# Optimization experiments

Hardware: AMD Instinct MI355X
Metric: run time of the kernel (lower is better)

## Reference

```python
import jax, jax.numpy as jnp
import numpy as np

N, F, DEG, C = 20000, 64, 16, 16   # nodes, features, in-degree incl. self loop, classes
E = N * (DEG - 1)                   # regular (non-self-loop) edges


def setup_inputs() -> dict:
    key = jax.random.key(0)
    ks = jax.random.split(key, 12)
    x = jax.random.normal(ks[0], (N, F), dtype=jnp.float32)
    src = jax.random.randint(ks[1], (E,), 0, N, dtype=jnp.int32)
    dst = jnp.repeat(jnp.arange(N, dtype=jnp.int32), DEG - 1)  # exactly DEG-1 in-edges/node
    edge_index = jnp.stack([src, dst])
    s = 1.0 / np.sqrt(F)
    params = {}
    for i, kw, kb in ((1, ks[2], ks[3]), (2, ks[4], ks[5]), (3, ks[6], ks[7])):
        params[f"W{i}"] = jax.random.normal(kw, (F, F), dtype=jnp.float32) * s
        params[f"b{i}"] = jax.random.normal(kb, (F,), dtype=jnp.float32) * s
    params["Wfc"] = jax.random.normal(ks[8], (C, F), dtype=jnp.float32) * s
    params["bfc"] = jax.random.normal(ks[9], (C,), dtype=jnp.float32) * s
    return {"x": x, "edge_index": edge_index, **params}


def _pca_conv(h, src, dst, W, b):
    # GCNConv.forward: linear first, then propagate with symmetric normalization.
    hl = h @ W.T                                             # [N, F]
    # add self loops (appended after regular edges, as in PyG)
    loop = jnp.arange(N, dtype=src.dtype)
    src_a = jnp.concatenate([src, loop])
    dst_a = jnp.concatenate([dst, loop])
    deg = jnp.zeros((N,), hl.dtype).at[dst_a].add(1.0)
    dinv = jax.lax.rsqrt(deg)
    norm = dinv[src_a] * dinv[dst_a]                         # [Ea]
    m = norm[:, None] * hl[src_a]                            # messages [Ea, F]
    # aggregate(): pack each destination's messages contiguously, in edge order
    order = jnp.argsort(dst_a)                               # stable sort by destination
    sd = dst_a[order]
    slot = jnp.arange(sd.shape[0]) - jnp.searchsorted(sd, sd, side='left')
    neigh = jnp.zeros((N, DEG, F), hl.dtype).at[sd, slot].set(m[order])
    neigh = neigh.reshape(N, DEG * F)                        # [N, max_degree*F]
    # torch.pca_lowrank(neigh, q=F, center=True): top-F right singular vectors of
    # the column-centered matrix; computed via eigh on the (DEG*F x DEG*F) Gram.
    Xc = neigh - jnp.mean(neigh, axis=0, keepdims=True)
    G = Xc.T @ Xc                                            # [DEG*F, DEG*F]
    _, V = jnp.linalg.eigh(G)                                # ascending eigenvalues
    Vtop = V[:, ::-1][:, :F]                                 # top-F principal directions
    proj = neigh @ Vtop                                      # note: projects UNcentered neigh
    return proj @ W.T + b                                    # self.lin again + bias


def reference(x, edge_index, W1, b1, W2, b2, W3, b3, Wfc, bfc):
    src, dst = edge_index[0], edge_index[1]
    h = jax.nn.relu(_pca_conv(x, src, dst, W1, b1))
    h = jax.nn.relu(_pca_conv(h, src, dst, W2, b2))
    h = jax.nn.relu(_pca_conv(h, src, dst, W3, b3))
    out = h @ Wfc.T + bfc
    return jax.nn.log_softmax(out, axis=-1)
```

## Files before the change

kernel.cpp:

```cpp
#include <hip/hip_runtime.h>
#include <cmath>

#define NNODES 20000
#define FD 64
#define EPN 15
#define NB 1024
#define BSUB 80
#define NCLS 16

__global__ __launch_bounds__(256) void k_linT(const float* __restrict__ X,
    const float* __restrict__ W, const float* __restrict__ bias,
    float* __restrict__ out, int ncol, int relu)
{
  __shared__ float Wsh[64][65];
  __shared__ float Xsh[64][65];
  int t = threadIdx.x;
  int r0 = blockIdx.x * 64;
  for (int idx = t; idx < ncol * 64; idx += 256) Wsh[idx >> 6][idx & 63] = W[idx];
  for (int idx = t; idx < 64 * 64; idx += 256) {
    int r = idx >> 6, c = idx & 63;
    Xsh[r][c] = (r0 + r < NNODES) ? X[(size_t)(r0 + r) * 64 + c] : 0.f;
  }
  __syncthreads();
  for (int idx = t; idx < 64 * ncol; idx += 256) {
    int r = idx / ncol, o = idx % ncol;
    float acc = 0.f;
    #pragma unroll
    for (int j = 0; j < 64; j++) acc += Xsh[r][j] * Wsh[o][j];
    if (bias) acc += bias[o];
    if (relu) acc = fmaxf(acc, 0.f);
    if (r0 + r < NNODES) out[(size_t)(r0 + r) * ncol + o] = acc;
  }
}

__global__ __launch_bounds__(256) void k_meanslot(const float* __restrict__ hl,
    const int* __restrict__ src, float* __restrict__ mus)
{
  int k = blockIdx.x;
  int part = blockIdx.y;
  int t = threadIdx.x;
  int c = t & 63, sub = t >> 6;
  int d0 = part * 2500;
  float acc = 0.f;
  for (int d = d0 + sub; d < d0 + 2500; d += 4) {
    int row = (k < EPN) ? src[d * EPN + k] : d;
    acc += hl[(size_t)row * 64 + c];
  }
  __shared__ float red[4][64];
  red[sub][c] = acc;
  __syncthreads();
  if (t < 64) {
    float s = red[0][t] + red[1][t] + red[2][t] + red[3][t];
    atomicAdd(&mus[k * 64 + t], s * (1.f / 20000.f));
  }
}

__global__ __launch_bounds__(256) void k_gram(const float* __restrict__ hl,
    const int* __restrict__ src, const float* __restrict__ mus,
    float* __restrict__ T)
{
  __shared__ float Ash[64][64];
  __shared__ float Bsh[64][64];
  __shared__ float muA[64], muB[64];
  int t = threadIdx.x;
  int pr = blockIdx.x, i = 0, rem = pr;
  for (int ii = 0; ii < 16; ii++) {
    int cnt = 16 - ii;
    if (rem < cnt) { i = ii; break; }
    rem -= cnt;
  }
  int j = i + rem;
  if (t < 64) muA[t] = mus[i * 64 + t];
  else if (t < 128) muB[t - 64] = mus[j * 64 + (t - 64)];
  float acc[4][4] = {};
  int a0 = (t & 15) * 4, b0 = (t >> 4) * 4;
  int d0 = blockIdx.y * 4000, d1 = d0 + 4000;
  for (int dc = d0; dc < d1; dc += 64) {
    __syncthreads();
    for (int item = t; item < 1024; item += 256) {
      int rr = item >> 4, f4 = item & 15;
      int d = dc + rr;
      float4 va = make_float4(0.f, 0.f, 0.f, 0.f);
      float4 vb = va;
      if (d < d1) {
        int ra = (i < EPN) ? src[d * EPN + i] : d;
        int rb = (j < EPN) ? src[d * EPN + j] : d;
        va = ((const float4*)hl)[(size_t)ra * 16 + f4];
        vb = ((const float4*)hl)[(size_t)rb * 16 + f4];
        int cb = f4 * 4;
        va.x -= muA[cb]; va.y -= muA[cb + 1]; va.z -= muA[cb + 2]; va.w -= muA[cb + 3];
        vb.x -= muB[cb]; vb.y -= muB[cb + 1]; vb.z -= muB[cb + 2]; vb.w -= muB[cb + 3];
      }
      ((float4*)&Ash[rr][0])[f4] = va;
      ((float4*)&Bsh[rr][0])[f4] = vb;
    }
    __syncthreads();
    for (int dd = 0; dd < 64; dd++) {
      float av[4], bv[4];
      #pragma unroll
      for (int u = 0; u < 4; u++) av[u] = Ash[dd][a0 + u];
      #pragma unroll
      for (int u = 0; u < 4; u++) bv[u] = Bsh[dd][b0 + u];
      #pragma unroll
      for (int x = 0; x < 4; x++)
        #pragma unroll
        for (int y = 0; y < 4; y++) acc[x][y] += av[x] * bv[y];
    }
  }
  #pragma unroll
  for (int x = 0; x < 4; x++)
    #pragma unroll
    for (int y = 0; y < 4; y++)
      atomicAdd(&T[(size_t)(i * 64 + a0 + x) * NB + (j * 64 + b0 + y)], acc[x][y]);
}

__global__ __launch_bounds__(256) void k_assembleG(const float* __restrict__ T,
    float* __restrict__ G)
{
  size_t idx = (size_t)blockIdx.x * 256 + threadIdx.x;
  int p = (int)(idx >> 10), q = (int)(idx & 1023);
  int ti = p >> 6, tj = q >> 6;
  float v = (ti <= tj) ? T[idx] : T[((size_t)q << 10) | (size_t)p];
  G[idx] = v * (1.f / 256.f);
}

__global__ __launch_bounds__(256) void k_gemmG2(const float* __restrict__ G,
    float* __restrict__ G2)
{
  __shared__ float Ash[64][68];
  __shared__ float Bsh[64][68];
  int t = threadIdx.x;
  int bi = blockIdx.x * 64, bj = blockIdx.y * 64;
  int a0 = (t & 15) * 4, b0 = (t >> 4) * 4;
  float acc[4][4] = {};
  for (int d0 = 0; d0 < NB; d0 += 64) {
    __syncthreads();
    for (int item = t; item < 1024; item += 256) {
      int rr = item >> 4, f4 = item & 15;
      *(float4*)&Ash[rr][f4 * 4] =
          ((const float4*)G)[(size_t)(d0 + rr) * 256 + (bi >> 2) + f4];
      *(float4*)&Bsh[rr][f4 * 4] =
          ((const float4*)G)[(size_t)(d0 + rr) * 256 + (bj >> 2) + f4];
    }
    __syncthreads();
    for (int dd = 0; dd < 64; dd++) {
      float av[4], bv[4];
      #pragma unroll
      for (int u = 0; u < 4; u++) av[u] = Ash[dd][a0 + u];
      #pragma unroll
      for (int u = 0; u < 4; u++) bv[u] = Bsh[dd][b0 + u];
      #pragma unroll
      for (int x = 0; x < 4; x++)
        #pragma unroll
        for (int y = 0; y < 4; y++) acc[x][y] += av[x] * bv[y];
    }
  }
  #pragma unroll
  for (int x = 0; x < 4; x++) {
    float4 v = make_float4(acc[x][0], acc[x][1], acc[x][2], acc[x][3]);
    ((float4*)G2)[(size_t)(bi + a0 + x) * 256 + ((bj + b0) >> 2)] = v;
  }
}

__global__ void k_cut0(const float* __restrict__ G, double* __restrict__ scal)
{
  __shared__ float red[256];
  float m = 0.f;
  for (int p = threadIdx.x; p < NB; p += 256) m = fmaxf(m, G[(size_t)p * NB + p]);
  red[threadIdx.x] = m;
  __syncthreads();
  for (int s = 128; s; s >>= 1) {
    if (threadIdx.x < s) red[threadIdx.x] = fmaxf(red[threadIdx.x], red[threadIdx.x + s]);
    __syncthreads();
  }
  if (threadIdx.x == 0) {
    double c = 0.9 * (double)red[0];
    scal[0] = c;
    scal[1] = c * c;
  }
}

__global__ void k_initS(float* __restrict__ S)
{
  int idx = blockIdx.x * 256 + threadIdx.x;
  if (idx < NB * BSUB) {
    unsigned u = (unsigned)(idx + 1) * 2654435761u;
    u ^= u >> 16; u *= 2246822519u; u ^= u >> 13; u *= 3266489917u; u ^= u >> 16;
    S[idx] = ((float)u * (1.f / 4294967296.f)) - 0.5f;
  }
}

__global__ __launch_bounds__(256) void k_gzfused(const float* __restrict__ G,
    const float* __restrict__ Z, const float* __restrict__ Zp,
    float* __restrict__ P, float* __restrict__ out, int* __restrict__ cnt,
    const double* __restrict__ cptr, float s1, float s2, float s3)
{
  __shared__ float Gs[32][68];
  __shared__ float Zs[64][84];
  __shared__ int lastf;
  int t = threadIdx.x;
  int r0b = blockIdx.x;
  int r0 = r0b * 32;
  int kz = blockIdx.y;
  int cg = t & 15, rg = t >> 4;
  float acc0[5] = {}, acc1[5] = {};
  for (int k0 = kz * 128; k0 < kz * 128 + 128; k0 += 64) {
    __syncthreads();
    #pragma unroll
    for (int s = 0; s < 2; s++) {
      int item = t + s * 256;
      int rr = item >> 4, f4 = item & 15;
      float4 g = ((const float4*)G)[(size_t)(r0 + rr) * 256 + (k0 >> 2) + f4];
      *(float4*)&Gs[rr][f4 * 4] = g;
    }
    #pragma unroll
    for (int s = 0; s < 5; s++) {
      int item = t + s * 256;
      int rr = item / 20, f4 = item % 20;
      float4 z = ((const float4*)Z)[(size_t)(k0 + rr) * 20 + f4];
      *(float4*)&Zs[rr][f4 * 4] = z;
    }
    __syncthreads();
    for (int kk = 0; kk < 64; kk++) {
      float g0 = Gs[rg * 2 + 0][kk];
      float g1 = Gs[rg * 2 + 1][kk];
      float z[5];
      #pragma unroll
      for (int m = 0; m < 5; m++) z[m] = Zs[kk][cg * 5 + m];
      #pragma unroll
      for (int m = 0; m < 5; m++) { acc0[m] += g0 * z[m]; acc1[m] += g1 * z[m]; }
    }
  }
  size_t base = (size_t)kz * (NB * BSUB) + (size_t)(r0 + rg * 2) * BSUB + cg * 5;
  #pragma unroll
  for (int m = 0; m < 5; m++) P[base + m] = acc0[m];
  #pragma unroll
  for (int m = 0; m < 5; m++) P[base + BSUB + m] = acc1[m];
  __threadfence();
  __syncthreads();
  if (t == 0) {
    int old = atomicAdd(&cnt[r0b], 1);
    lastf = (old == 7) ? 1 : 0;
  }
  __syncthreads();
  if (!lastf) return;
  __threadfence();
  float coef = s1;
  if (cptr) coef = s1 * (float)(2.0 / cptr[0]);
  const float4* P4 = (const float4*)P;
  for (int idx = t; idx < 640; idx += 256) {
    size_t o4 = (size_t)r0 * 20 + idx;
    float4 a = P4[o4];
    #pragma unroll
    for (int u = 1; u < 8; u++) {
      float4 b = P4[(size_t)u * 20480 + o4];
      a.x += b.x; a.y += b.y; a.z += b.z; a.w += b.w;
    }
    float4 z = ((const float4*)Z)[o4];
    float4 o;
    o.x = coef * a.x + s2 * z.x;
    o.y = coef * a.y + s2 * z.y;
    o.z = coef * a.z + s2 * z.z;
    o.w = coef * a.w + s2 * z.w;
    if (s3 != 0.f) {
      float4 zp = ((const float4*)Zp)[o4];
      o.x += s3 * zp.x; o.y += s3 * zp.y; o.z += s3 * zp.z; o.w += s3 * zp.w;
    }
    ((float4*)out)[o4] = o;
  }
  __syncthreads();
  if (t == 0) cnt[r0b] = 0;
}

__global__ void k_syrk(const float* __restrict__ S, double* __restrict__ C)
{
  int idx = blockIdx.x * 256 + threadIdx.x;
  if (idx >= BSUB * BSUB) return;
  int a = idx / BSUB, b = idx % BSUB;
  double acc = 0.0;
  for (int i = 0; i < NB; i++)
    acc += (double)S[(size_t)i * BSUB + a] * (double)S[(size_t)i * BSUB + b];
  C[idx] = acc;
}

__global__ void k_xty(const float* __restrict__ X, const float* __restrict__ Y,
                      float* __restrict__ M)
{
  int idx = blockIdx.x * 256 + threadIdx.x;
  if (idx >= BSUB * BSUB) return;
  int a = idx / BSUB, b = idx % BSUB;
  double acc = 0.0;
  for (int i = 0; i < NB; i++)
    acc += (double)X[(size_t)i * BSUB + a] * (double)Y[(size_t)i * BSUB + b];
  M[idx] = (float)acc;
}

__global__ __launch_bounds__(512) void k_cholinv(const double* __restrict__ Cin,
    float* __restrict__ Rinv)
{
  __shared__ double R[BSUB][BSUB + 1];
  __shared__ double rownew[2][BSUB];
  __shared__ double dinv[BSUB];
  __shared__ float X[BSUB][BSUB + 1];
  int t = threadIdx.x;
  for (int idx = t; idx < BSUB * BSUB; idx += 512)
    R[idx / BSUB][idx % BSUB] = Cin[idx];
  __syncthreads();
  double flr0 = 1e-30 * (fabs(R[0][0]) + 1e-280);
  int prevrow = -1;
  int pb = 0;
  int k = 0;
  while (k < BSUB - 1) {
    int nrem = BSUB - 1 - k;
    int total = (nrem * (nrem + 1)) >> 1;
    int cplen = (prevrow >= 0) ? (BSUB - prevrow) : 0;
    double piv = R[k][k];
    if (piv < flr0) piv = flr0;
    double rp = 1.0 / piv;
    bool pair = (k + 1 < BSUB - 1);
    if (pair) {
      double dk1 = R[k][k + 1];
      double p1 = R[k + 1][k + 1] - dk1 * dk1 * rp;
      if (p1 < flr0) p1 = flr0;
      double rp1 = 1.0 / p1;
      for (int idx = t; idx < total + cplen; idx += 512) {
        if (idx < total) {
          float nf = 2.f * (float)nrem + 1.f;
          int a = (int)((nf - sqrtf(nf * nf - 8.f * (float)idx)) * 0.5f);
          while (a > 0 && a * nrem - ((a * (a - 1)) >> 1) > idx) a--;
          while ((a + 1) * nrem - (((a + 1) * a) >> 1) <= idx) a++;
          int off = idx - (a * nrem - ((a * (a - 1)) >> 1));
          int i2 = k + 1 + a, j2 = i2 + off;
          if (a == 0) {
            rownew[pb][j2] = R[k + 1][j2] - dk1 * R[k][j2] * rp;
          } else {
            double v = R[i2][j2] - R[k][i2] * R[k][j2] * rp;
            double R1i = R[k + 1][i2] - dk1 * R[k][i2] * rp;
            double R1j = R[k + 1][j2] - dk1 * R[k][j2] * rp;
            v -= R1i * R1j * rp1;
            R[i2][j2] = v;
          }
        } else {
          int j = prevrow + (idx - total);
          R[prevrow][j] = rownew[pb ^ 1][j];
        }
      }
      __syncthreads();
      prevrow = k + 1; pb ^= 1; k += 2;
    } else {
      for (int idx = t; idx < total + cplen; idx += 512) {
        if (idx < total) {
          float nf = 2.f * (float)nrem + 1.f;
          int a = (int)((nf - sqrtf(nf * nf - 8.f * (float)idx)) * 0.5f);
          while (a > 0 && a * nrem - ((a * (a - 1)) >> 1) > idx) a--;
          while ((a + 1) * nrem - (((a + 1) * a) >> 1) <= idx) a++;
          int off = idx - (a * nrem - ((a * (a - 1)) >> 1));
          int i2 = k + 1 + a, j2 = i2 + off;
          R[i2][j2] -= R[k][i2] * R[k][j2] * rp;
        } else {
          int j = prevrow + (idx - total);
          R[prevrow][j] = rownew[pb ^ 1][j];
        }
      }
      __syncthreads();
      prevrow = -1; k += 1;
    }
  }
  if (prevrow >= 0) {
    for (int j = prevrow + t; j < BSUB; j += 512) R[prevrow][j] = rownew[pb ^ 1][j];
    __syncthreads();
  }
  if (t < BSUB) {
    double piv = R[t][t];
    if (piv < flr0) piv = flr0;
    dinv[t] = 1.0 / sqrt(piv);
  }
  __syncthreads();
  for (int idx = t; idx < BSUB * BSUB; idx += 512) {
    int kk = idx / BSUB, j = idx % BSUB;
    if (j > kk) R[kk][j] *= dinv[kk];
  }
  __syncthreads();
  if (t < BSUB) R[t][t] = 1.0 / dinv[t];
  __syncthreads();
  if (t < BSUB) {
    int j = t;
    X[j][j] = (float)dinv[j];
    for (int i = j - 1; i >= 0; i--) {
      double s = 0.0;
      for (int k2 = i + 1; k2 <= j; k2++) s += R[i][k2] * (double)X[k2][j];
      X[i][j] = (float)(-s * dinv[i]);
    }
    for (int i = j + 1; i < BSUB; i++) X[i][j] = 0.f;
  }
  __syncthreads();
  for (int idx = t; idx < BSUB * BSUB; idx += 512)
    Rinv[idx] = X[idx / BSUB][idx % BSUB];
}

__global__ __launch_bounds__(256) void k_gemmSR(const float* __restrict__ S,
    const float* __restrict__ Rinv, float* __restrict__ out)
{
  __shared__ float Rsh[BSUB][84];
  int t = threadIdx.x;
  for (int idx = t; idx < BSUB * BSUB; idx += 256)
    Rsh[idx / BSUB][idx % BSUB] = Rinv[idx];
  __syncthreads();
  int r0 = blockIdx.x * 32;
  int r = t >> 3, c0 = (t & 7) * 10;
  float acc[10] = {};
  const float* srow = &S[(size_t)(r0 + r) * BSUB];
  for (int k = 0; k < BSUB; k++) {
    float s = srow[k];
    #pragma unroll
    for (int m = 0; m < 10; m++) acc[m] += s * Rsh[k][c0 + m];
  }
  #pragma unroll
  for (int m = 0; m < 10; m++) out[(size_t)(r0 + r) * BSUB + c0 + m] = acc[m];
}

__global__ __launch_bounds__(1024) void k_jacobi(const float* __restrict__ Min,
    float* __restrict__ Uout, int* __restrict__ perm,
    double* __restrict__ cutout, int sweeps, int withU)
{
  __shared__ float Mb[2][BSUB][BSUB + 1];
  __shared__ float Ut[BSUB][BSUB];
  __shared__ float cs[2][40], sn[2][40];
  __shared__ int pp[2][40], qq[2][40];
  __shared__ float th[BSUB];
  __shared__ int id[BSUB];
  int t = threadIdx.x;
  for (int idx = t; idx < BSUB * BSUB; idx += 1024) {
    int i2 = idx / BSUB, j2 = idx % BSUB;
    Mb[0][i2][j2] = 0.5f * (Min[i2 * BSUB + j2] + Min[j2 * BSUB + i2]);
    if (withU) Ut[i2][j2] = (i2 == j2) ? 1.f : 0.f;
  }
  __syncthreads();
  int nrounds = sweeps * (BSUB - 1);
  int mcur = 0;
  for (int it = 0; it < nrounds; it++) {
    int r = it % (BSUB - 1);
    int pb = it & 1;
    float (*Mc)[BSUB + 1] = Mb[mcur];
    float (*Mn)[BSUB + 1] = Mb[mcur ^ 1];
    if (t < 40) {
      int p = (t == 0) ? 0 : 1 + (t - 1 + r) % (BSUB - 1);
      int q = 1 + (BSUB - 2 - t + r) % (BSUB - 1);
      if (p > q) { int tmp = p; p = q; q = tmp; }
      pp[pb][t] = p; qq[pb][t] = q;
      float apq = Mc[p][q];
      float c = 1.f, s = 0.f;
      if (fabsf(apq) > 1e-28f) {
        float tau = (Mc[q][q] - Mc[p][p]) / (2.f * apq);
        float tt = copysignf(1.f, tau) / (fabsf(tau) + sqrtf(1.f + tau * tau));
        c = rsqrtf(1.f + tt * tt);
        s = tt * c;
      }
      cs[pb][t] = c; sn[pb][t] = s;
    } else if (withU && it > 0) {
      int ob = pb ^ 1;
      for (int idx = t - 40; idx < 40 * 40; idx += 984) {
        unsigned pr = ((unsigned)idx * 3277u) >> 17;
        int m = idx - (int)pr * 40;
        int p = pp[ob][pr], q = qq[ob][pr];
        float c = cs[ob][pr], s = sn[ob][pr];
        float2 up = *(float2*)&Ut[p][2 * m];
        float2 uq = *(float2*)&Ut[q][2 * m];
        float2 np, nq;
        np.x = c * up.x - s * uq.x;  np.y = c * up.y - s * uq.y;
        nq.x = s * up.x + c * uq.x;  nq.y = s * up.y + c * uq.y;
        *(float2*)&Ut[p][2 * m] = np;
        *(float2*)&Ut[q][2 * m] = nq;
      }
    }
    __syncthreads();
    for (int idx = t; idx < 40 * 40; idx += 1024) {
      unsigned pr = ((unsigned)idx * 3277u) >> 17;
      int j = idx - (int)pr * 40;
      int p = pp[pb][pr], q = qq[pb][pr];
      float c = cs[pb][pr], s = sn[pb][pr];
      int k = pp[pb][j], k2 = qq[pb][j];
      float cj = cs[pb][j], sj = sn[pb][j];
      float mpk = Mc[p][k],  mqk = Mc[q][k];
      float mpk2 = Mc[p][k2], mqk2 = Mc[q][k2];
      float rpk  = c * mpk  - s * mqk;
      float rqk  = s * mpk  + c * mqk;
      float rpk2 = c * mpk2 - s * mqk2;
      float rqk2 = s * mpk2 + c * mqk2;
      Mn[p][k]  = cj * rpk - sj * rpk2;
      Mn[q][k]  = cj * rqk - sj * rqk2;
      Mn[p][k2] = sj * rpk + cj * rpk2;
      Mn[q][k2] = sj * rqk + cj * rqk2;
    }
    __syncthreads();
    mcur ^= 1;
  }
  if (withU) {
    int ob = (nrounds - 1) & 1;
    for (int idx = t; idx < 40 * 40; idx += 1024) {
      unsigned pr = ((unsigned)idx * 3277u) >> 17;
      int m = idx - (int)pr * 40;
      int p = pp[ob][pr], q = qq[ob][pr];
      float c = cs[ob][pr], s = sn[ob][pr];
      float2 up = *(float2*)&Ut[p][2 * m];
      float2 uq = *(float2*)&Ut[q][2 * m];
      float2 np, nq;
      np.x = c * up.x - s * uq.x;  np.y = c * up.y - s * uq.y;
      nq.x = s * up.x + c * uq.x;  nq.y = s * up.y + c * uq.y;
      *(float2*)&Ut[p][2 * m] = np;
      *(float2*)&Ut[q][2 * m] = nq;
    }
    __syncthreads();
  }
  float (*Mf)[BSUB + 1] = Mb[mcur];
  if (t < BSUB) { th[t] = Mf[t][t]; id[t] = t; }
  __syncthreads();
  if (t == 0) {
    for (int a = 1; a < BSUB; a++) {
      float v = th[a]; int ii = id[a]; int b = a - 1;
      while (b >= 0 && th[b] < v) { th[b + 1] = th[b]; id[b + 1] = id[b]; b--; }
      th[b + 1] = v; id[b + 1] = ii;
    }
    double cut = (double)th[BSUB - 1];
    double lo = 0.02 * (double)th[0];
    if (cut < lo) cut = lo;
    double hi = 0.98 * (double)th[63];
    if (cut > hi) cut = hi;
    cutout[0] = cut;
    cutout[1] = cut * cut;
  }
  __syncthreads();
  if (t < BSUB) perm[t] = id[t];
  if (withU)
    for (int idx = t; idx < BSUB * BSUB; idx += 1024) {
      int k = idx / BSUB, p = idx % BSUB;
      Uout[idx] = Ut[p][k];
    }
}

__global__ __launch_bounds__(256) void k_compose(const float* __restrict__ S,
    const float* __restrict__ U, const int* __restrict__ perm,
    float* __restrict__ out)
{
  __shared__ float Ush[BSUB][65];
  int t = threadIdx.x;
  for (int idx = t; idx < BSUB * 64; idx += 256) {
    int jj = idx >> 6, c = idx & 63;
    Ush[jj][c] = U[jj * BSUB + perm[c]];
  }
  __syncthreads();
  int r0 = blockIdx.x * 64;
  for (int oidx = t; oidx < 64 * 64; oidx += 256) {
    int r = oidx >> 6, c = oidx & 63;
    float acc = 0.f;
    const float* srow = &S[(size_t)(r0 + r) * BSUB];
    #pragma unroll 8
    for (int j = 0; j < BSUB; j++) acc += srow[j] * Ush[j][c];
    out[(size_t)(r0 + r) * 64 + c] = acc;
  }
}

__global__ __launch_bounds__(256) void k_projlin(const float* __restrict__ hl,
    const int* __restrict__ src, const float* __restrict__ Vtop,
    const float* __restrict__ W, const float* __restrict__ bias,
    float* __restrict__ hout)
{
  __shared__ float Vsh[64][68];
  __shared__ float Hsh[64][68];
  __shared__ float Psh[64][68];
  int t = threadIdx.x;
  int d0 = blockIdx.x * 64;
  int dd = t & 63, pg = t >> 6;
  float acc[16] = {};
  for (int k = 0; k < 16; k++) {
    __syncthreads();
    for (int item = t; item < 1024; item += 256) {
      int rr = item >> 4, f4 = item & 15;
      *(float4*)&Vsh[rr][f4 * 4] = ((const float4*)Vtop)[(size_t)(k * 64 + rr) * 16 + f4];
      int d = d0 + rr;
      float4 v = make_float4(0.f, 0.f, 0.f, 0.f);
      if (d < NNODES) {
        int row = (k < EPN) ? src[d * EPN + k] : d;
        v = ((const float4*)hl)[(size_t)row * 16 + f4];
      }
      *(float4*)&Hsh[rr][f4 * 4] = v;
    }
    __syncthreads();
    for (int j = 0; j < 64; j++) {
      float h = Hsh[dd][j];
      #pragma unroll
      for (int m = 0; m < 16; m++) acc[m] += h * Vsh[j][pg * 16 + m];
    }
  }
  __syncthreads();
  #pragma unroll
  for (int m = 0; m < 16; m++) Psh[dd][pg * 16 + m] = acc[m] * (1.f / 16.f);
  for (int item = t; item < 1024; item += 256) {
    int rr = item >> 4, f4 = item & 15;
    *(float4*)&Vsh[rr][f4 * 4] = ((const float4*)W)[(size_t)rr * 16 + f4];
  }
  __syncthreads();
  if (d0 + dd < NNODES) {
    #pragma unroll
    for (int m = 0; m < 16; m++) {
      int o = pg * 16 + m;
      float a = bias[o];
      for (int j = 0; j < 64; j++) a += Psh[dd][j] * Vsh[o][j];
      hout[(size_t)(d0 + dd) * 64 + o] = fmaxf(a, 0.f);
    }
  }
}

__global__ void k_logsoftmax(const float* __restrict__ logits, float* __restrict__ out)
{
  int n = blockIdx.x * 256 + threadIdx.x;
  if (n >= NNODES) return;
  float v[NCLS];
  float mx = -1e30f;
  #pragma unroll
  for (int c = 0; c < NCLS; c++) { v[c] = logits[(size_t)n * NCLS + c]; mx = fmaxf(mx, v[c]); }
  float se = 0.f;
  #pragma unroll
  for (int c = 0; c < NCLS; c++) se += expf(v[c] - mx);
  float lse = mx + logf(se);
  #pragma unroll
  for (int c = 0; c < NCLS; c++) out[(size_t)n * NCLS + c] = v[c] - lse;
}

extern "C" void kernel_launch(void* const* d_in, const int* in_sizes, int n_in,
                              void* d_out, int out_size, void* d_ws, size_t ws_size,
                              hipStream_t stream)
{
  (void)in_sizes; (void)n_in; (void)out_size; (void)ws_size;
  const float* x = (const float*)d_in[0];
  const int* src = (const int*)d_in[1];
  const float* Wl[3] = { (const float*)d_in[2], (const float*)d_in[4], (const float*)d_in[6] };
  const float* bl[3] = { (const float*)d_in[3], (const float*)d_in[5], (const float*)d_in[7] };
  const float* Wfc = (const float*)d_in[8];
  const float* bfc = (const float*)d_in[9];
  float* outp = (float*)d_out;

  char* w = (char*)d_ws;
  auto alloc = [&](size_t bytes) -> char* {
    char* p = w; w += (bytes + 255) & ~(size_t)255; return p;
  };
  float* hA   = (float*)alloc((size_t)NNODES * 64 * 4);
  float* hB   = (float*)alloc((size_t)NNODES * 64 * 4);
  float* hl   = (float*)alloc((size_t)NNODES * 64 * 4);
  float* T    = (float*)alloc((size_t)NB * NB * 4);
  float* G    = (float*)alloc((size_t)NB * NB * 4);
  float* G2   = (float*)alloc((size_t)NB * NB * 4);
  float* mus  = (float*)alloc(16 * 64 * 4);
  float* Zb[6];
  for (int i = 0; i < 6; i++) Zb[i] = (float*)alloc((size_t)NB * BSUB * 4);
  float* P     = (float*)alloc((size_t)8 * NB * BSUB * 4);
  int* cnt     = (int*)alloc(32 * 4);
  double* C    = (double*)alloc(BSUB * BSUB * 8);
  float* Rinv  = (float*)alloc(BSUB * BSUB * 4);
  float* Mm    = (float*)alloc(BSUB * BSUB * 4);
  float* U     = (float*)alloc(BSUB * BSUB * 4);
  int* perm    = (int*)alloc(BSUB * 4);
  float* Vtop  = (float*)alloc((size_t)NB * 64 * 4);
  double* scal = (double*)alloc(16 * 8);

  const int GRID_ROWS = (NNODES + 63) / 64;

  hipMemsetAsync(cnt, 0, 32 * 4, stream);

  int cur = 0;
  auto gemmGZ = [&](const float* A, const float* Z, const float* Zp, float* o,
                    const double* cptr, float s1, float s2, float s3) {
    hipLaunchKernelGGL(k_gzfused, dim3(32, 8), dim3(256), 0, stream,
                       A, Z, Zp, P, o, cnt, cptr, s1, s2, s3);
  };
  auto chunk2 = [&](int deg, const double* cptr) {
    int a = (cur + 1) % 6, b = (cur + 2) % 6;
    float* bufs[3] = { Zb[cur], Zb[a], Zb[b] };
    int ip = 0, ic = 0, io = 1;
    for (int s = 0; s < deg; s++) {
      if (s == 0)
        gemmGZ(G2, bufs[ic], nullptr, bufs[io], cptr, 1.f, -1.f, 0.f);
      else
        gemmGZ(G2, bufs[ic], bufs[ip], bufs[io], cptr, 2.f, -2.f, -1.f);
      if (s == 0) { ip = 0; ic = 1; io = 2; }
      else { int tmp = ip; ip = ic; ic = io; io = tmp; }
    }
    int sel = (deg - 1) % 3;
    cur = (sel == 0) ? a : (sel == 1) ? b : cur;
  };
  auto cholqr = [&]() {
    hipLaunchKernelGGL(k_syrk, dim3(25), dim3(256), 0, stream, Zb[cur], C);
    hipLaunchKernelGGL(k_cholinv, dim3(1), dim3(512), 0, stream, C, Rinv);
    int o = (cur + 1) % 6;
    hipLaunchKernelGGL(k_gemmSR, dim3(32), dim3(256), 0, stream, Zb[cur], Rinv, Zb[o]);
    cur = o;
  };
  auto rrmid = [&](double* cutp) {
    int y = (cur + 1) % 6;
    gemmGZ(G, Zb[cur], nullptr, Zb[y], nullptr, 1.f, 0.f, 0.f);
    hipLaunchKernelGGL(k_xty, dim3(25), dim3(256), 0, stream, Zb[cur], Zb[y], Mm);
    hipLaunchKernelGGL(k_jacobi, dim3(1), dim3(1024), 0, stream,
                       Mm, U, perm, cutp, 2, 0);
  };
  auto rrfinal = [&](double* cutp) {
    int y = (cur + 1) % 6;
    gemmGZ(G, Zb[cur], nullptr, Zb[y], nullptr, 1.f, 0.f, 0.f);
    hipLaunchKernelGGL(k_xty, dim3(25), dim3(256), 0, stream, Zb[cur], Zb[y], Mm);
    hipLaunchKernelGGL(k_jacobi, dim3(1), dim3(1024), 0, stream,
                       Mm, U, perm, cutp, 5, 1);
    hipLaunchKernelGGL(k_compose, dim3(16), dim3(256), 0, stream,
                       Zb[cur], U, perm, Vtop);
  };

  const float* hin = x;
  float* hout = hA;
  for (int l = 0; l < 3; l++) {
    hipLaunchKernelGGL(k_linT, dim3(GRID_ROWS), dim3(256), 0, stream,
                       hin, Wl[l], (const float*)nullptr, hl, 64, 0);
    hipMemsetAsync(mus, 0, 16 * 64 * 4, stream);
    hipLaunchKernelGGL(k_meanslot, dim3(16, 8), dim3(256), 0, stream, hl, src, mus);
    hipMemsetAsync(T, 0, (size_t)NB * NB * 4, stream);
    hipLaunchKernelGGL(k_gram, dim3(136, 5), dim3(256), 0, stream, hl, src, mus, T);
    hipLaunchKernelGGL(k_assembleG, dim3(4096), dim3(256), 0, stream, T, G);
    hipLaunchKernelGGL(k_cut0, dim3(1), dim3(256), 0, stream, G, scal);
    hipLaunchKernelGGL(k_gemmG2, dim3(16, 16), dim3(256), 0, stream, G, G2);
    cur = 0;
    hipLaunchKernelGGL(k_initS, dim3((NB * BSUB + 255) / 256), dim3(256), 0, stream, Zb[cur]);
    chunk2(6, &scal[1]); cholqr();
    rrmid(&scal[2]);
    chunk2(7, &scal[3]); cholqr();
    chunk2(7, &scal[3]); cholqr();
    rrfinal(&scal[4]);
    hipLaunchKernelGGL(k_projlin, dim3(GRID_ROWS), dim3(256), 0, stream,
                       hl, src, Vtop, Wl[l], bl[l], hout);
    hin = hout;
    hout = (hout == hA) ? hB : hA;
  }
  hipLaunchKernelGGL(k_linT, dim3(GRID_ROWS), dim3(256), 0, stream,
                     hin, Wfc, bfc, hl, NCLS, 0);
  hipLaunchKernelGGL(k_logsoftmax, dim3((NNODES + 255) / 256), dim3(256), 0, stream,
                     hl, outp);
}
```

Before: 9.791 ms.

## Materialize centered neighbor matrix and compute Gram via split-K SYRK; streamline Jacobi

Adds a path that builds the centered neighbor matrix X (N x 1024) explicitly, then computes its Gram matrix with a 128x128-tiled register-blocked SYRK. The node dimension is split 16 ways into partial buffers, which are summed afterwards; no memset or atomics are needed. Separately, the Jacobi eigen kernel packs rotation data into float4, computes the pair indices incrementally and unrolls the per-thread work assignment, removing modulo and division work from every round. The new Gram path needs about 80MB of X plus 64MB of partials in workspace and falls back to the old path if ws_size is too small.

New measurement: 9.352 ms. 4.5% less time.

```diff
diff --git a/kernel.cpp b/kernel.cpp
--- a/kernel.cpp
+++ b/kernel.cpp
@@ -7,6 +7,7 @@
 #define NB 1024
 #define BSUB 80
 #define NCLS 16
+#define SYRK_SPLIT 16
 
 __global__ __launch_bounds__(256) void k_linT(const float* __restrict__ X,
     const float* __restrict__ W, const float* __restrict__ bias,
@@ -53,6 +54,95 @@
     float s = red[0][t] + red[1][t] + red[2][t] + red[3][t];
     atomicAdd(&mus[k * 64 + t], s * (1.f / 20000.f));
   }
+}
+
+__global__ __launch_bounds__(256) void k_buildX(const float* __restrict__ hl,
+    const int* __restrict__ src, const float* __restrict__ mus,
+    float* __restrict__ X)
+{
+  __shared__ float4 mu4[256];
+  int t = threadIdx.x;
+  int d0 = blockIdx.x * 64;
+  mu4[t] = ((const float4*)mus)[t];
+  __syncthreads();
+  for (int k = 0; k < 16; k++) {
+    for (int item = t; item < 1024; item += 256) {
+      int rr = item >> 4, f4 = item & 15;
+      int d = d0 + rr;
+      if (d < NNODES) {
+        int row = (k < EPN) ? src[d * EPN + k] : d;
+        float4 v = ((const float4*)hl)[(size_t)row * 16 + f4];
+        float4 m = mu4[k * 16 + f4];
+        v.x -= m.x; v.y -= m.y; v.z -= m.z; v.w -= m.w;
+        ((float4*)X)[(size_t)d * 256 + k * 16 + f4] = v;
+      }
+    }
+  }
+}
+
+__global__ __launch_bounds__(256) void k_syrkX(const float* __restrict__ X,
+    float* __restrict__ TP)
+{
+  __shared__ float As[32][128];
+  __shared__ float Bs[32][128];
+  int t = threadIdx.x;
+  int pr = blockIdx.x, I = 0, rem = pr;
+  for (int ii = 0; ii < 8; ii++) {
+    int cnt = 8 - ii;
+    if (rem < cnt) { I = ii; break; }
+    rem -= cnt;
+  }
+  int J = I + rem;
+  int d0 = blockIdx.y * (NNODES / SYRK_SPLIT);
+  int d1 = d0 + (NNODES / SYRK_SPLIT);
+  int a0 = (t & 15) * 8, b0 = (t >> 4) * 8;
+  float acc[8][8] = {};
+  for (int dc = d0; dc < d1; dc += 32) {
+    __syncthreads();
+    for (int item = t; item < 1024; item += 256) {
+      int rr = item >> 5, c4 = item & 31;
+      int d = dc + rr;
+      float4 va = make_float4(0.f, 0.f, 0.f, 0.f), vb = va;
+      if (d < d1) {
+        va = ((const float4*)X)[(size_t)d * 256 + I * 32 + c4];
+        vb = ((const float4*)X)[(size_t)d * 256 + J * 32 + c4];
+      }
+      *(float4*)&As[rr][c4 * 4] = va;
+      *(float4*)&Bs[rr][c4 * 4] = vb;
+    }
+    __syncthreads();
+    for (int dd = 0; dd < 32; dd++) {
+      float av[8], bv[8];
+      *(float4*)&av[0] = *(const float4*)&As[dd][a0];
+      *(float4*)&av[4] = *(const float4*)&As[dd][a0 + 4];
+      *(float4*)&bv[0] = *(const float4*)&Bs[dd][b0];
+      *(float4*)&bv[4] = *(const float4*)&Bs[dd][b0 + 4];
+      #pragma unroll
+      for (int x = 0; x < 8; x++)
+        #pragma unroll
+        for (int y = 0; y < 8; y++) acc[x][y] += av[x] * bv[y];
+    }
+  }
+  float* Tout = TP + (size_t)blockIdx.y * ((size_t)NB * NB);
+  #pragma unroll
+  for (int x = 0; x < 8; x++) {
+    size_t base = (size_t)(I * 128 + a0 + x) * NB + (J * 128 + b0);
+    *(float4*)&Tout[base]     = make_float4(acc[x][0], acc[x][1], acc[x][2], acc[x][3]);
+    *(float4*)&Tout[base + 4] = make_float4(acc[x][4], acc[x][5], acc[x][6], acc[x][7]);
+  }
+}
+
+__global__ __launch_bounds__(256) void k_assembleG16(const float* __restrict__ TP,
+    float* __restrict__ G)
+{
+  size_t idx = (size_t)blockIdx.x * 256 + threadIdx.x;
+  int p = (int)(idx >> 10), q = (int)(idx & 1023);
+  int ti = p >> 6, tj = q >> 6;
+  size_t e = (ti <= tj) ? idx : (((size_t)q << 10) | (size_t)p);
+  float v = 0.f;
+  #pragma unroll
+  for (int s2 = 0; s2 < 16; s2++) v += TP[(size_t)s2 * ((size_t)NB * NB) + e];
+  G[idx] = v * (1.f / 256.f);
 }
 
 __global__ __launch_bounds__(256) void k_gram(const float* __restrict__ hl,
@@ -425,8 +515,7 @@
 {
   __shared__ float Mb[2][BSUB][BSUB + 1];
   __shared__ float Ut[BSUB][BSUB];
-  __shared__ float cs[2][40], sn[2][40];
-  __shared__ int pp[2][40], qq[2][40];
+  __shared__ float4 rot[2][40];
   __shared__ float th[BSUB];
   __shared__ int id[BSUB];
   int t = threadIdx.x;
@@ -435,19 +524,33 @@
     Mb[0][i2][j2] = 0.5f * (Min[i2 * BSUB + j2] + Min[j2 * BSUB + i2]);
     if (withU) Ut[i2][j2] = (i2 == j2) ? 1.f : 0.f;
   }
+  int pr0 = t / 40, j0 = t - pr0 * 40;
+  int pr1 = -1, j1 = 0;
+  {
+    int i1 = t + 1024;
+    if (i1 < 1600) { pr1 = i1 / 40; j1 = i1 - pr1 * 40; }
+  }
+  int upr0 = -1, um0 = 0, upr1 = -1, um1 = 0;
+  if (t >= 40) {
+    int u0 = t - 40;              upr0 = u0 / 40; um0 = u0 - upr0 * 40;
+    int u1 = t - 40 + 984;
+    if (u1 < 1600) { upr1 = u1 / 40; um1 = u1 - upr1 * 40; }
+  }
+  int rp_ = 0, rq_ = 0;
+  if (t < 40) {
+    rp_ = (t == 0) ? 0 : 1 + (t - 1) % 79;
+    rq_ = 1 + (78 - t) % 79;
+  }
   __syncthreads();
   int nrounds = sweeps * (BSUB - 1);
   int mcur = 0;
   for (int it = 0; it < nrounds; it++) {
-    int r = it % (BSUB - 1);
     int pb = it & 1;
     float (*Mc)[BSUB + 1] = Mb[mcur];
     float (*Mn)[BSUB + 1] = Mb[mcur ^ 1];
     if (t < 40) {
-      int p = (t == 0) ? 0 : 1 + (t - 1 + r) % (BSUB - 1);
-      int q = 1 + (BSUB - 2 - t + r) % (BSUB - 1);
+      int p = rp_, q = rq_;
       if (p > q) { int tmp = p; p = q; q = tmp; }
-      pp[pb][t] = p; qq[pb][t] = q;
       float apq = Mc[p][q];
       float c = 1.f, s = 0.f;
       if (fabsf(apq) > 1e-28f) {
@@ -456,31 +559,44 @@
         c = rsqrtf(1.f + tt * tt);
         s = tt * c;
       }
-      cs[pb][t] = c; sn[pb][t] = s;
+      rot[pb][t] = make_float4(c, s, __int_as_float(p), __int_as_float(q));
+      if (t > 0) rp_ = (rp_ == 79) ? 1 : rp_ + 1;
+      rq_ = (rq_ == 79) ? 1 : rq_ + 1;
     } else if (withU && it > 0) {
       int ob = pb ^ 1;
-      for (int idx = t - 40; idx < 40 * 40; idx += 984) {
-        unsigned pr = ((unsigned)idx * 3277u) >> 17;
-        int m = idx - (int)pr * 40;
-        int p = pp[ob][pr], q = qq[ob][pr];
-        float c = cs[ob][pr], s = sn[ob][pr];
-        float2 up = *(float2*)&Ut[p][2 * m];
-        float2 uq = *(float2*)&Ut[q][2 * m];
+      {
+        float4 R0 = rot[ob][upr0];
+        int p = __float_as_int(R0.z), q = __float_as_int(R0.w);
+        float c = R0.x, s = R0.y;
+        float2 up = *(float2*)&Ut[p][2 * um0];
+        float2 uq = *(float2*)&Ut[q][2 * um0];
         float2 np, nq;
         np.x = c * up.x - s * uq.x;  np.y = c * up.y - s * uq.y;
         nq.x = s * up.x + c * uq.x;  nq.y = s * up.y + c * uq.y;
-        *(float2*)&Ut[p][2 * m] = np;
-        *(float2*)&Ut[q][2 * m] = nq;
+        *(float2*)&Ut[p][2 * um0] = np;
+        *(float2*)&Ut[q][2 * um0] = nq;
       }
-    }
-    __syncthreads();
-    for (int idx = t; idx < 40 * 40; idx += 1024) {
-      unsigned pr = ((unsigned)idx * 3277u) >> 17;
-      int j = idx - (int)pr * 40;
-      int p = pp[pb][pr], q = qq[pb][pr];
-      float c = cs[pb][pr], s = sn[pb][pr];
-      int k = pp[pb][j], k2 = qq[pb][j];
-      float cj = cs[pb][j], sj = sn[pb][j];
+      if (upr1 >= 0) {
+        float4 R1 = rot[ob][upr1];
+        int p = __float_as_int(R1.z), q = __float_as_int(R1.w);
+        float c = R1.x, s = R1.y;
+        float2 up = *(float2*)&Ut[p][2 * um1];
+        float2 uq = *(float2*)&Ut[q][2 * um1];
+        float2 np, nq;
+        np.x = c * up.x - s * uq.x;  np.y = c * up.y - s * uq.y;
+        nq.x = s * up.x + c * uq.x;  nq.y = s * up.y + c * uq.y;
+        *(float2*)&Ut[p][2 * um1] = np;
+        *(float2*)&Ut[q][2 * um1] = nq;
+      }
+    }
+    __syncthreads();
+    {
+      float4 Rp = rot[pb][pr0];
+      float4 Rj = rot[pb][j0];
+      int p = __float_as_int(Rp.z), q = __float_as_int(Rp.w);
+      float c = Rp.x, s = Rp.y;
+      int k = __float_as_int(Rj.z), k2 = __float_as_int(Rj.w);
+      float cj = Rj.x, sj = Rj.y;
       float mpk = Mc[p][k],  mqk = Mc[q][k];
       float mpk2 = Mc[p][k2], mqk2 = Mc[q][k2];
       float rpk  = c * mpk  - s * mqk;
@@ -492,23 +608,52 @@
       Mn[p][k2] = sj * rpk + cj * rpk2;
       Mn[q][k2] = sj * rqk + cj * rqk2;
     }
+    if (pr1 >= 0) {
+      float4 Rp = rot[pb][pr1];
+      float4 Rj = rot[pb][j1];
+      int p = __float_as_int(Rp.z), q = __float_as_int(Rp.w);
+      float c = Rp.x, s = Rp.y;
+      int k = __float_as_int(Rj.z), k2 = __float_as_int(Rj.w);
+      float cj = Rj.x, sj = Rj.y;
+      float mpk = Mc[p][k],  mqk = Mc[q][k];
+      float mpk2 = Mc[p][k2], mqk2 = Mc[q][k2];
+      float rpk  = c * mpk  - s * mqk;
+      float rqk  = s * mpk  + c * mqk;
+      float rpk2 = c * mpk2 - s * mqk2;
+      float rqk2 = s * mpk2 + c * mqk2;
+      Mn[p][k]  = cj * rpk - sj * rpk2;
+      Mn[q][k]  = cj * rqk - sj * rqk2;
+      Mn[p][k2] = sj * rpk + cj * rpk2;
+      Mn[q][k2] = sj * rqk + cj * rqk2;
+    }
     __syncthreads();
     mcur ^= 1;
   }
   if (withU) {
     int ob = (nrounds - 1) & 1;
-    for (int idx = t; idx < 40 * 40; idx += 1024) {
-      unsigned pr = ((unsigned)idx * 3277u) >> 17;
-      int m = idx - (int)pr * 40;
-      int p = pp[ob][pr], q = qq[ob][pr];
-      float c = cs[ob][pr], s = sn[ob][pr];
-      float2 up = *(float2*)&Ut[p][2 * m];
-      float2 uq = *(float2*)&Ut[q][2 * m];
+    {
+      float4 R0 = rot[ob][pr0];
+      int p = __float_as_int(R0.z), q = __float_as_int(R0.w);
+      float c = R0.x, s = R0.y;
+      float2 up = *(float2*)&Ut[p][2 * j0];
+      float2 uq = *(float2*)&Ut[q][2 * j0];
       float2 np, nq;
       np.x = c * up.x - s * uq.x;  np.y = c * up.y - s * uq.y;
       nq.x = s * up.x + c * uq.x;  nq.y = s * up.y + c * uq.y;
-      *(float2*)&Ut[p][2 * m] = np;
-      *(float2*)&Ut[q][2 * m] = nq;
+      *(float2*)&Ut[p][2 * j0] = np;
+      *(float2*)&Ut[q][2 * j0] = nq;
+    }
+    if (pr1 >= 0) {
+      float4 R1 = rot[ob][pr1];
+      int p = __float_as_int(R1.z), q = __float_as_int(R1.w);
+      float c = R1.x, s = R1.y;
+      float2 up = *(float2*)&Ut[p][2 * j1];
+      float2 uq = *(float2*)&Ut[q][2 * j1];
+      float2 np, nq;
+      np.x = c * up.x - s * uq.x;  np.y = c * up.y - s * uq.y;
+      nq.x = s * up.x + c * uq.x;  nq.y = s * up.y + c * uq.y;
+      *(float2*)&Ut[p][2 * j1] = np;
+      *(float2*)&Ut[q][2 * j1] = nq;
     }
     __syncthreads();
   }
@@ -631,7 +776,7 @@
                               void* d_out, int out_size, void* d_ws, size_t ws_size,
                               hipStream_t stream)
 {
-  (void)in_sizes; (void)n_in; (void)out_size; (void)ws_size;
+  (void)in_sizes; (void)n_in; (void)out_size;
   const float* x = (const float*)d_in[0];
   const int* src = (const int*)d_in[1];
   const float* Wl[3] = { (const float*)d_in[2], (const float*)d_in[4], (const float*)d_in[6] };
@@ -662,6 +807,10 @@
   int* perm    = (int*)alloc(BSUB * 4);
   float* Vtop  = (float*)alloc((size_t)NB * 64 * 4);
   double* scal = (double*)alloc(16 * 8);
+  float* X  = (float*)alloc((size_t)NNODES * NB * 4);
+  float* TP = (float*)alloc((size_t)SYRK_SPLIT * (size_t)NB * NB * 4);
+  size_t used = (size_t)(w - (char*)d_ws);
+  int fastg = (used <= ws_size) ? 1 : 0;
 
   const int GRID_ROWS = (NNODES + 63) / 64;
 
@@ -719,9 +868,16 @@
                        hin, Wl[l], (const float*)nullptr, hl, 64, 0);
     hipMemsetAsync(mus, 0, 16 * 64 * 4, stream);
     hipLaunchKernelGGL(k_meanslot, dim3(16, 8), dim3(256), 0, stream, hl, src, mus);
-    hipMemsetAsync(T, 0, (size_t)NB * NB * 4, stream);
-    hipLaunchKernelGGL(k_gram, dim3(136, 5), dim3(256), 0, stream, hl, src, mus, T);
-    hipLaunchKernelGGL(k_assembleG, dim3(4096), dim3(256), 0, stream, T, G);
+    if (fastg) {
+      hipLaunchKernelGGL(k_buildX, dim3(GRID_ROWS), dim3(256), 0, stream,
+                         hl, src, mus, X);
+      hipLaunchKernelGGL(k_syrkX, dim3(36, SYRK_SPLIT), dim3(256), 0, stream, X, TP);
+      hipLaunchKernelGGL(k_assembleG16, dim3(4096), dim3(256), 0, stream, TP, G);
+    } else {
+      hipMemsetAsync(T, 0, (size_t)NB * NB * 4, stream);
+      hipLaunchKernelGGL(k_gram, dim3(136, 5), dim3(256), 0, stream, hl, src, mus, T);
+      hipLaunchKernelGGL(k_assembleG, dim3(4096), dim3(256), 0, stream, T, G);
+    }
     hipLaunchKernelGGL(k_cut0, dim3(1), dim3(256), 0, stream, G, scal);
     hipLaunchKernelGGL(k_gemmG2, dim3(16, 16), dim3(256), 0, stream, G, G2);
     cur = 0;
```
